# Kernel tuning notes

Hardware: AMD Instinct MI355X
Metric: run time of the kernel (lower is better)

## Reference

```python
import jax, jax.numpy as jnp
import numpy as np

N = 8192
NFEAT = 512
NHID = 256
NCLASS = 40
EDGE_P = 0.002  # ~16 avg degree


def setup_inputs() -> dict:
    key = jax.random.key(0)
    k1, k2, k3, k4 = jax.random.split(key, 4)
    x = jax.random.normal(k1, (N, NFEAT), dtype=jnp.float32)
    # unnormalized binary adjacency without self loops (module adds eye itself)
    adj = (jax.random.uniform(k2, (N, N)) < EDGE_P).astype(jnp.float32)
    # GCNConv weights: torch.rand(in, out) -> uniform[0,1)
    W1 = jax.random.uniform(k3, (NFEAT, NHID), dtype=jnp.float32)
    W2 = jax.random.uniform(k4, (NHID, NCLASS), dtype=jnp.float32)
    return {"x": x, "adj": adj, "W1": W1, "W2": W2}


def reference(x, adj, W1, W2):
    n = adj.shape[0]
    # add self loops: in_adj.to_dense() + eye
    A_hat = adj + jnp.eye(n, dtype=adj.dtype)
    # normalize_adj: D^{-1/2} A_hat D^{-1/2} (diag matmuls == row/col scaling)
    d = A_hat.sum(-1) ** -0.5  # [N]
    norm_adj = d[:, None] * A_hat * d[None, :]
    # conv1: relu(adj @ x @ W1); dropout is identity in eval mode
    h = jax.nn.relu((norm_adj @ x) @ W1)
    # conv2 reuses the same normalized adjacency (only one DGG layer by default)
    h2 = jax.nn.relu((norm_adj @ h) @ W2)
    return jax.nn.log_softmax(h2, axis=-1)
```

## Files before the change

### kernel.cpp

```cpp
#include <hip/hip_runtime.h>
#include <math.h>

#define NV 8192
#define CAP 64

typedef __attribute__((ext_vector_type(8))) short short8;
typedef __attribute__((ext_vector_type(4))) float f32x4;

static __device__ __forceinline__ unsigned short f2bf(float v) {
  unsigned int u = __float_as_uint(v);
  unsigned int r = (u + 0x7fffu + ((u >> 16) & 1u)) >> 16;
  return (unsigned short)r;
}
static __device__ __forceinline__ float bf2f(unsigned short h) {
  return __uint_as_float(((unsigned int)h) << 16);
}

__global__ __launch_bounds__(256) void mega_build_gemm1(
    const float* __restrict__ adj, const float* __restrict__ x,
    const float* __restrict__ W1, int* __restrict__ cols,
    int* __restrict__ rowcount, float* __restrict__ dinv,
    float* __restrict__ diagv, float* __restrict__ XW1) {
  __shared__ __align__(16) unsigned short sAh[128][40];
  __shared__ __align__(16) unsigned short sAl[128][40];
  __shared__ __align__(16) unsigned short sBh[64][40];
  __shared__ __align__(16) unsigned short sBl[64][40];
  __shared__ int cnt;
  __shared__ int diag_nz;
  __shared__ int wsum[4];

  int t = threadIdx.x;
  int lane = t & 63;

  if (blockIdx.x < 256) {
    const int K = 512;
    int b = blockIdx.x;
    int bn = (b & 3) * 64;
    int bm = (b >> 2) * 128;
    int w = t >> 6;
    int quad = lane >> 4, m16 = lane & 15;
    f32x4 acc[2][4] = {};
    for (int k0 = 0; k0 < K; k0 += 32) {
#pragma unroll
      for (int i = 0; i < 4; i++) {
        int id = t + i * 256;
        int row = id >> 3;
        int fq = id & 7;
        float4 v = *(const float4*)&x[(size_t)(bm + row) * K + k0 + fq * 4];
        ushort4 h, l;
        h.x = f2bf(v.x); l.x = f2bf(v.x - bf2f(h.x));
        h.y = f2bf(v.y); l.y = f2bf(v.y - bf2f(h.y));
        h.z = f2bf(v.z); l.z = f2bf(v.z - bf2f(h.z));
        h.w = f2bf(v.w); l.w = f2bf(v.w - bf2f(h.w));
        *(ushort4*)&sAh[row][fq * 4] = h;
        *(ushort4*)&sAl[row][fq * 4] = l;
      }
#pragma unroll
      for (int j = 0; j < 2; j++) {
        int id = t + j * 256;
        int k = id >> 4;
        int n4 = (id & 15) * 4;
        float4 v = *(const float4*)&W1[(size_t)(k0 + k) * 256 + bn + n4];
        float va[4] = {v.x, v.y, v.z, v.w};
#pragma unroll
        for (int c = 0; c < 4; c++) {
          unsigned short h = f2bf(va[c]);
          sBh[n4 + c][k] = h;
          sBl[n4 + c][k] = f2bf(va[c] - bf2f(h));
        }
      }
      __syncthreads();
      short8 ah[2], al[2], bh[4], bl[4];
#pragma unroll
      for (int i = 0; i < 2; i++) {
        ah[i] = *(const short8*)&sAh[w * 32 + i * 16 + m16][quad * 8];
        al[i] = *(const short8*)&sAl[w * 32 + i * 16 + m16][quad * 8];
      }
#pragma unroll
      for (int j = 0; j < 4; j++) {
        bh[j] = *(const short8*)&sBh[j * 16 + m16][quad * 8];
        bl[j] = *(const short8*)&sBl[j * 16 + m16][quad * 8];
      }
#pragma unroll
      for (int i = 0; i < 2; i++)
#pragma unroll
        for (int j = 0; j < 4; j++) {
          acc[i][j] = __builtin_amdgcn_mfma_f32_16x16x32_bf16(ah[i], bh[j], acc[i][j], 0, 0, 0);
          acc[i][j] = __builtin_amdgcn_mfma_f32_16x16x32_bf16(al[i], bh[j], acc[i][j], 0, 0, 0);
          acc[i][j] = __builtin_amdgcn_mfma_f32_16x16x32_bf16(ah[i], bl[j], acc[i][j], 0, 0, 0);
        }
      __syncthreads();
    }
#pragma unroll
    for (int i = 0; i < 2; i++)
#pragma unroll
      for (int j = 0; j < 4; j++)
#pragma unroll
        for (int r = 0; r < 4; r++)
          XW1[(size_t)(bm + w * 32 + i * 16 + quad * 4 + r) * 256 + bn + j * 16 + m16] =
              acc[i][j][r];
  } else {
    int row = blockIdx.x - 256;
    if (t == 0) { cnt = 0; diag_nz = 0; }
    __syncthreads();
    const float4* arow = (const float4*)(adj + (size_t)row * NV);
    float4 v0 = arow[t + 0 * 256];
    float4 v1 = arow[t + 1 * 256];
    float4 v2 = arow[t + 2 * 256];
    float4 v3 = arow[t + 3 * 256];
    float4 v4 = arow[t + 4 * 256];
    float4 v5 = arow[t + 5 * 256];
    float4 v6 = arow[t + 6 * 256];
    float4 v7 = arow[t + 7 * 256];
    int mycount = 0;
    float4 vv[8] = {v0, v1, v2, v3, v4, v5, v6, v7};
#pragma unroll
    for (int u = 0; u < 8; u++) {
      int i = t + u * 256;
      float va[4] = {vv[u].x, vv[u].y, vv[u].z, vv[u].w};
#pragma unroll
      for (int j = 0; j < 4; j++) {
        bool nz = (va[j] != 0.0f);
        mycount += nz ? 1 : 0;
        int c = i * 4 + j;
        bool isdiag = nz && (c == row);
        bool take = nz && !isdiag;
        if (isdiag) diag_nz = 1;
        unsigned long long m = __ballot(take);
        if (m != 0ull) {
          int tot = __popcll(m);
          int pre = __popcll(m & ((1ull << lane) - 1ull));
          int leader = __ffsll((unsigned long long)m) - 1;
          int base = 0;
          if (lane == leader) base = atomicAdd(&cnt, tot);
          base = __shfl(base, leader, 64);
          if (take) {
            int p = base + pre;
            if (p < CAP) cols[(size_t)row * CAP + p] = c;
          }
        }
      }
    }
    for (int off = 32; off > 0; off >>= 1) mycount += __shfl_xor(mycount, off, 64);
    if (lane == 0) wsum[t >> 6] = mycount;
    __syncthreads();
    if (t == 0) {
      int nnz = wsum[0] + wsum[1] + wsum[2] + wsum[3];
      float deg = (float)nnz + 1.0f;
      dinv[row] = 1.0f / sqrtf(deg);
      diagv[row] = diag_nz ? 2.0f : 1.0f;
      rowcount[row] = cnt > CAP ? CAP : cnt;
    }
  }
}

__global__ __launch_bounds__(256) void spmm_relu_k(
    const float* __restrict__ Z, const int* __restrict__ cols,
    const int* __restrict__ rowcount, const float* __restrict__ dinv,
    const float* __restrict__ diagv, float* __restrict__ H) {
  int lane = threadIdx.x & 63;
  int row = blockIdx.x * 4 + (threadIdx.x >> 6);
  const float4* Zr = (const float4*)Z;
  float di = dinv[row];
  float4 z = Zr[(size_t)row * 64 + lane];
  float dd = diagv[row] * di;
  float4 acc;
  acc.x = dd * z.x; acc.y = dd * z.y; acc.z = dd * z.z; acc.w = dd * z.w;
  int cnt = rowcount[row];
  const int* cr = cols + (size_t)row * CAP;
  int e = 0;
  for (; e + 8 <= cnt; e += 8) {
    int c0 = cr[e + 0], c1 = cr[e + 1], c2 = cr[e + 2], c3 = cr[e + 3];
    int c4 = cr[e + 4], c5 = cr[e + 5], c6 = cr[e + 6], c7 = cr[e + 7];
    float w0 = dinv[c0], w1 = dinv[c1], w2 = dinv[c2], w3 = dinv[c3];
    float w4 = dinv[c4], w5 = dinv[c5], w6 = dinv[c6], w7 = dinv[c7];
    float4 g0 = Zr[(size_t)c0 * 64 + lane];
    float4 g1 = Zr[(size_t)c1 * 64 + lane];
    float4 g2 = Zr[(size_t)c2 * 64 + lane];
    float4 g3 = Zr[(size_t)c3 * 64 + lane];
    float4 g4 = Zr[(size_t)c4 * 64 + lane];
    float4 g5 = Zr[(size_t)c5 * 64 + lane];
    float4 g6 = Zr[(size_t)c6 * 64 + lane];
    float4 g7 = Zr[(size_t)c7 * 64 + lane];
    acc.x += w0 * g0.x + w1 * g1.x + w2 * g2.x + w3 * g3.x;
    acc.y += w0 * g0.y + w1 * g1.y + w2 * g2.y + w3 * g3.y;
    acc.z += w0 * g0.z + w1 * g1.z + w2 * g2.z + w3 * g3.z;
    acc.w += w0 * g0.w + w1 * g1.w + w2 * g2.w + w3 * g3.w;
    acc.x += w4 * g4.x + w5 * g5.x + w6 * g6.x + w7 * g7.x;
    acc.y += w4 * g4.y + w5 * g5.y + w6 * g6.y + w7 * g7.y;
    acc.z += w4 * g4.z + w5 * g5.z + w6 * g6.z + w7 * g7.z;
    acc.w += w4 * g4.w + w5 * g5.w + w6 * g6.w + w7 * g7.w;
  }
  for (; e + 4 <= cnt; e += 4) {
    int c0 = cr[e + 0], c1 = cr[e + 1], c2 = cr[e + 2], c3 = cr[e + 3];
    float w0 = dinv[c0], w1 = dinv[c1], w2 = dinv[c2], w3 = dinv[c3];
    float4 g0 = Zr[(size_t)c0 * 64 + lane];
    float4 g1 = Zr[(size_t)c1 * 64 + lane];
    float4 g2 = Zr[(size_t)c2 * 64 + lane];
    float4 g3 = Zr[(size_t)c3 * 64 + lane];
    acc.x += w0 * g0.x + w1 * g1.x + w2 * g2.x + w3 * g3.x;
    acc.y += w0 * g0.y + w1 * g1.y + w2 * g2.y + w3 * g3.y;
    acc.z += w0 * g0.z + w1 * g1.z + w2 * g2.z + w3 * g3.z;
    acc.w += w0 * g0.w + w1 * g1.w + w2 * g2.w + w3 * g3.w;
  }
  for (; e < cnt; e++) {
    int c = cr[e];
    float w = dinv[c];
    float4 g = Zr[(size_t)c * 64 + lane];
    acc.x += w * g.x; acc.y += w * g.y; acc.z += w * g.z; acc.w += w * g.w;
  }
  float4 o;
  o.x = fmaxf(acc.x * di, 0.0f);
  o.y = fmaxf(acc.y * di, 0.0f);
  o.z = fmaxf(acc.z * di, 0.0f);
  o.w = fmaxf(acc.w * di, 0.0f);
  ((float4*)H)[(size_t)row * 64 + lane] = o;
}

__global__ __launch_bounds__(256) void gemm2_mfma(
    const float* __restrict__ H, const float* __restrict__ W2,
    float* __restrict__ HW2) {
  const int K = 256;
  __shared__ __align__(16) unsigned short sAh[32][40];
  __shared__ __align__(16) unsigned short sAl[32][40];
  __shared__ __align__(16) unsigned short sBh[64][40];
  __shared__ __align__(16) unsigned short sBl[64][40];
  int t = threadIdx.x;
  int bm = blockIdx.x * 32;
  int lane = t & 63, w = t >> 6;
  int quad = lane >> 4, m16 = lane & 15;
  int i = w & 1;
  int jj = (w >> 1) * 2;
  f32x4 acc[2] = {};
  for (int k0 = 0; k0 < K; k0 += 32) {
    {
      int row = t >> 3;
      int fq = t & 7;
      float4 v = *(const float4*)&H[(size_t)(bm + row) * K + k0 + fq * 4];
      ushort4 h, l;
      h.x = f2bf(v.x); l.x = f2bf(v.x - bf2f(h.x));
      h.y = f2bf(v.y); l.y = f2bf(v.y - bf2f(h.y));
      h.z = f2bf(v.z); l.z = f2bf(v.z - bf2f(h.z));
      h.w = f2bf(v.w); l.w = f2bf(v.w - bf2f(h.w));
      *(ushort4*)&sAh[row][fq * 4] = h;
      *(ushort4*)&sAl[row][fq * 4] = l;
    }
#pragma unroll
    for (int j = 0; j < 2; j++) {
      int id = t + j * 256;
      int k = id >> 4;
      int n4 = (id & 15) * 4;
#pragma unroll
      for (int c = 0; c < 4; c++) {
        float v = (n4 + c < 40) ? W2[(size_t)(k0 + k) * 40 + n4 + c] : 0.0f;
        unsigned short h = f2bf(v);
        sBh[n4 + c][k] = h;
        sBl[n4 + c][k] = f2bf(v - bf2f(h));
      }
    }
    __syncthreads();
    short8 ah = *(const short8*)&sAh[i * 16 + m16][quad * 8];
    short8 al = *(const short8*)&sAl[i * 16 + m16][quad * 8];
#pragma unroll
    for (int jx = 0; jx < 2; jx++) {
      short8 bh = *(const short8*)&sBh[(jj + jx) * 16 + m16][quad * 8];
      short8 bl = *(const short8*)&sBl[(jj + jx) * 16 + m16][quad * 8];
      acc[jx] = __builtin_amdgcn_mfma_f32_16x16x32_bf16(ah, bh, acc[jx], 0, 0, 0);
      acc[jx] = __builtin_amdgcn_mfma_f32_16x16x32_bf16(al, bh, acc[jx], 0, 0, 0);
      acc[jx] = __builtin_amdgcn_mfma_f32_16x16x32_bf16(ah, bl, acc[jx], 0, 0, 0);
    }
    __syncthreads();
  }
#pragma unroll
  for (int jx = 0; jx < 2; jx++)
#pragma unroll
    for (int r = 0; r < 4; r++)
      HW2[(size_t)(bm + i * 16 + quad * 4 + r) * 64 + (jj + jx) * 16 + m16] =
          acc[jx][r];
}

__global__ __launch_bounds__(256) void spmm2_lsm_k(
    const float* __restrict__ Z, const int* __restrict__ cols,
    const int* __restrict__ rowcount, const float* __restrict__ dinv,
    const float* __restrict__ diagv, float* __restrict__ out) {
  int lane = threadIdx.x & 63;
  int row = blockIdx.x * 4 + (threadIdx.x >> 6);
  float di = dinv[row];
  float acc = diagv[row] * di * Z[(size_t)row * 64 + lane];
  int cnt = rowcount[row];
  const int* cr = cols + (size_t)row * CAP;
  int e = 0;
  for (; e + 8 <= cnt; e += 8) {
    int c0 = cr[e + 0], c1 = cr[e + 1], c2 = cr[e + 2], c3 = cr[e + 3];
    int c4 = cr[e + 4], c5 = cr[e + 5], c6 = cr[e + 6], c7 = cr[e + 7];
    float w0 = dinv[c0], w1 = dinv[c1], w2 = dinv[c2], w3 = dinv[c3];
    float w4 = dinv[c4], w5 = dinv[c5], w6 = dinv[c6], w7 = dinv[c7];
    float g0 = Z[(size_t)c0 * 64 + lane];
    float g1 = Z[(size_t)c1 * 64 + lane];
    float g2 = Z[(size_t)c2 * 64 + lane];
    float g3 = Z[(size_t)c3 * 64 + lane];
    float g4 = Z[(size_t)c4 * 64 + lane];
    float g5 = Z[(size_t)c5 * 64 + lane];
    float g6 = Z[(size_t)c6 * 64 + lane];
    float g7 = Z[(size_t)c7 * 64 + lane];
    acc += w0 * g0 + w1 * g1 + w2 * g2 + w3 * g3;
    acc += w4 * g4 + w5 * g5 + w6 * g6 + w7 * g7;
  }
  for (; e + 4 <= cnt; e += 4) {
    int c0 = cr[e + 0], c1 = cr[e + 1], c2 = cr[e + 2], c3 = cr[e + 3];
    float w0 = dinv[c0], w1 = dinv[c1], w2 = dinv[c2], w3 = dinv[c3];
    acc += w0 * Z[(size_t)c0 * 64 + lane] + w1 * Z[(size_t)c1 * 64 + lane] +
           w2 * Z[(size_t)c2 * 64 + lane] + w3 * Z[(size_t)c3 * 64 + lane];
  }
  for (; e < cnt; e++) {
    int c = cr[e];
    acc += dinv[c] * Z[(size_t)c * 64 + lane];
  }
  float h2 = (lane < 40) ? fmaxf(acc * di, 0.0f) : -INFINITY;
  float m = h2;
  for (int off = 32; off > 0; off >>= 1) m = fmaxf(m, __shfl_xor(m, off, 64));
  float ex = (lane < 40) ? expf(h2 - m) : 0.0f;
  float s = ex;
  for (int off = 32; off > 0; off >>= 1) s += __shfl_xor(s, off, 64);
  float ls = logf(s);
  if (lane < 40) out[(size_t)row * 40 + lane] = h2 - m - ls;
}

extern "C" void kernel_launch(void* const* d_in, const int* in_sizes, int n_in,
                              void* d_out, int out_size, void* d_ws, size_t ws_size,
                              hipStream_t stream) {
  (void)in_sizes; (void)n_in; (void)out_size; (void)ws_size;
  const float* x   = (const float*)d_in[0];
  const float* adj = (const float*)d_in[1];
  const float* W1  = (const float*)d_in[2];
  const float* W2  = (const float*)d_in[3];
  float* out = (float*)d_out;
  char* ws = (char*)d_ws;

  int*   cols     = (int*)(ws);
  int*   rowcount = (int*)(ws + 2097152);
  float* dinv     = (float*)(ws + 2129920);
  float* diagv    = (float*)(ws + 2162688);
  float* XW1      = (float*)(ws + 2195456);
  float* H        = (float*)(ws + 10584064);
  float* HW2      = (float*)(ws + 18972672);

  hipLaunchKernelGGL(mega_build_gemm1, dim3(256 + NV), dim3(256), 0, stream,
                     adj, x, W1, cols, rowcount, dinv, diagv, XW1);
  hipLaunchKernelGGL(spmm_relu_k, dim3(NV / 4), dim3(256), 0, stream,
                     XW1, cols, rowcount, dinv, diagv, H);
  hipLaunchKernelGGL(gemm2_mfma, dim3(NV / 32), dim3(256), 0, stream,
                     H, W2, HW2);
  hipLaunchKernelGGL(spmm2_lsm_k, dim3(NV / 4), dim3(256), 0, stream,
                     HW2, cols, rowcount, dinv, diagv, out);
}
```

Measured before the change: 411.5 us.

## Halve GEMM1 tile height and replace per-element ballots with bitmask scan compaction

The XW1 GEMM now uses 64-row tiles instead of 128, doubling the GEMM block count to 512 and cutting LDS and register use per block. The adjacency row scan no longer does a ballot plus shuffle plus LDS atomic for each of the 32 elements per thread. Each thread instead builds a 32-bit mask of its nonzeros, a wave prefix scan gives its write offsets, and one atomic per wave reserves space. The degree is now taken from the compacted count plus the diagonal flag, and the order of column indices within a row changes.

```diff
diff --git a/kernel.cpp b/kernel.cpp
--- a/kernel.cpp
+++ b/kernel.cpp
@@ -21,28 +21,27 @@
     const float* __restrict__ W1, int* __restrict__ cols,
     int* __restrict__ rowcount, float* __restrict__ dinv,
     float* __restrict__ diagv, float* __restrict__ XW1) {
-  __shared__ __align__(16) unsigned short sAh[128][40];
-  __shared__ __align__(16) unsigned short sAl[128][40];
+  __shared__ __align__(16) unsigned short sAh[64][40];
+  __shared__ __align__(16) unsigned short sAl[64][40];
   __shared__ __align__(16) unsigned short sBh[64][40];
   __shared__ __align__(16) unsigned short sBl[64][40];
   __shared__ int cnt;
   __shared__ int diag_nz;
-  __shared__ int wsum[4];
 
   int t = threadIdx.x;
   int lane = t & 63;
 
-  if (blockIdx.x < 256) {
+  if (blockIdx.x < 512) {
     const int K = 512;
     int b = blockIdx.x;
     int bn = (b & 3) * 64;
-    int bm = (b >> 2) * 128;
+    int bm = (b >> 2) * 64;
     int w = t >> 6;
     int quad = lane >> 4, m16 = lane & 15;
-    f32x4 acc[2][4] = {};
+    f32x4 acc[4] = {};
     for (int k0 = 0; k0 < K; k0 += 32) {
 #pragma unroll
-      for (int i = 0; i < 4; i++) {
+      for (int i = 0; i < 2; i++) {
         int id = t + i * 256;
         int row = id >> 3;
         int fq = id & 7;
@@ -70,83 +69,74 @@
         }
       }
       __syncthreads();
-      short8 ah[2], al[2], bh[4], bl[4];
-#pragma unroll
-      for (int i = 0; i < 2; i++) {
-        ah[i] = *(const short8*)&sAh[w * 32 + i * 16 + m16][quad * 8];
-        al[i] = *(const short8*)&sAl[w * 32 + i * 16 + m16][quad * 8];
-      }
+      short8 ah = *(const short8*)&sAh[w * 16 + m16][quad * 8];
+      short8 al = *(const short8*)&sAl[w * 16 + m16][quad * 8];
 #pragma unroll
       for (int j = 0; j < 4; j++) {
-        bh[j] = *(const short8*)&sBh[j * 16 + m16][quad * 8];
-        bl[j] = *(const short8*)&sBl[j * 16 + m16][quad * 8];
-      }
-#pragma unroll
-      for (int i = 0; i < 2; i++)
-#pragma unroll
-        for (int j = 0; j < 4; j++) {
-          acc[i][j] = __builtin_amdgcn_mfma_f32_16x16x32_bf16(ah[i], bh[j], acc[i][j], 0, 0, 0);
-          acc[i][j] = __builtin_amdgcn_mfma_f32_16x16x32_bf16(al[i], bh[j], acc[i][j], 0, 0, 0);
-          acc[i][j] = __builtin_amdgcn_mfma_f32_16x16x32_bf16(ah[i], bl[j], acc[i][j], 0, 0, 0);
-        }
+        short8 bh = *(const short8*)&sBh[j * 16 + m16][quad * 8];
+        short8 bl = *(const short8*)&sBl[j * 16 + m16][quad * 8];
+        acc[j] = __builtin_amdgcn_mfma_f32_16x16x32_bf16(ah, bh, acc[j], 0, 0, 0);
+        acc[j] = __builtin_amdgcn_mfma_f32_16x16x32_bf16(al, bh, acc[j], 0, 0, 0);
+        acc[j] = __builtin_amdgcn_mfma_f32_16x16x32_bf16(ah, bl, acc[j], 0, 0, 0);
+      }
       __syncthreads();
     }
 #pragma unroll
-    for (int i = 0; i < 2; i++)
-#pragma unroll
-      for (int j = 0; j < 4; j++)
-#pragma unroll
-        for (int r = 0; r < 4; r++)
-          XW1[(size_t)(bm + w * 32 + i * 16 + quad * 4 + r) * 256 + bn + j * 16 + m16] =
-              acc[i][j][r];
+    for (int j = 0; j < 4; j++)
+#pragma unroll
+      for (int r = 0; r < 4; r++)
+        XW1[(size_t)(bm + w * 16 + quad * 4 + r) * 256 + bn + j * 16 + m16] =
+            acc[j][r];
   } else {
-    int row = blockIdx.x - 256;
+    int row = blockIdx.x - 512;
     if (t == 0) { cnt = 0; diag_nz = 0; }
     __syncthreads();
     const float4* arow = (const float4*)(adj + (size_t)row * NV);
-    float4 v0 = arow[t + 0 * 256];
-    float4 v1 = arow[t + 1 * 256];
-    float4 v2 = arow[t + 2 * 256];
-    float4 v3 = arow[t + 3 * 256];
-    float4 v4 = arow[t + 4 * 256];
-    float4 v5 = arow[t + 5 * 256];
-    float4 v6 = arow[t + 6 * 256];
-    float4 v7 = arow[t + 7 * 256];
-    int mycount = 0;
-    float4 vv[8] = {v0, v1, v2, v3, v4, v5, v6, v7};
+    float4 vv[8];
+    vv[0] = arow[t + 0 * 256];
+    vv[1] = arow[t + 1 * 256];
+    vv[2] = arow[t + 2 * 256];
+    vv[3] = arow[t + 3 * 256];
+    vv[4] = arow[t + 4 * 256];
+    vv[5] = arow[t + 5 * 256];
+    vv[6] = arow[t + 6 * 256];
+    vv[7] = arow[t + 7 * 256];
+    unsigned int wm = 0;
 #pragma unroll
     for (int u = 0; u < 8; u++) {
-      int i = t + u * 256;
       float va[4] = {vv[u].x, vv[u].y, vv[u].z, vv[u].w};
 #pragma unroll
       for (int j = 0; j < 4; j++) {
         bool nz = (va[j] != 0.0f);
-        mycount += nz ? 1 : 0;
-        int c = i * 4 + j;
-        bool isdiag = nz && (c == row);
-        bool take = nz && !isdiag;
-        if (isdiag) diag_nz = 1;
-        unsigned long long m = __ballot(take);
-        if (m != 0ull) {
-          int tot = __popcll(m);
-          int pre = __popcll(m & ((1ull << lane) - 1ull));
-          int leader = __ffsll((unsigned long long)m) - 1;
-          int base = 0;
-          if (lane == leader) base = atomicAdd(&cnt, tot);
-          base = __shfl(base, leader, 64);
-          if (take) {
-            int p = base + pre;
-            if (p < CAP) cols[(size_t)row * CAP + p] = c;
-          }
+        int c = 4 * t + (u << 10) + j;
+        if (nz) {
+          if (c == row) diag_nz = 1;
+          else wm |= 1u << (u * 4 + j);
         }
       }
     }
-    for (int off = 32; off > 0; off >>= 1) mycount += __shfl_xor(mycount, off, 64);
-    if (lane == 0) wsum[t >> 6] = mycount;
+    int myc = __popc(wm);
+    int pre = myc;
+#pragma unroll
+    for (int off = 1; off < 64; off <<= 1) {
+      int nb = __shfl_up(pre, off, 64);
+      if (lane >= off) pre += nb;
+    }
+    int wtot = __shfl(pre, 63, 64);
+    int base = 0;
+    if (lane == 63) base = atomicAdd(&cnt, wtot);
+    base = __shfl(base, 63, 64);
+    int p0 = base + (pre - myc);
+    while (wm) {
+      int p = __ffs(wm) - 1;
+      wm &= wm - 1;
+      int c = 4 * t + ((p >> 2) << 10) + (p & 3);
+      if (p0 < CAP) cols[(size_t)row * CAP + p0] = c;
+      p0++;
+    }
     __syncthreads();
     if (t == 0) {
-      int nnz = wsum[0] + wsum[1] + wsum[2] + wsum[3];
-      float deg = (float)nnz + 1.0f;
+      float deg = (float)(cnt + diag_nz) + 1.0f;
       dinv[row] = 1.0f / sqrtf(deg);
       diagv[row] = diag_nz ? 2.0f : 1.0f;
       rowcount[row] = cnt > CAP ? CAP : cnt;
@@ -345,7 +335,7 @@
   float* H        = (float*)(ws + 10584064);
   float* HW2      = (float*)(ws + 18972672);
 
-  hipLaunchKernelGGL(mega_build_gemm1, dim3(256 + NV), dim3(256), 0, stream,
+  hipLaunchKernelGGL(mega_build_gemm1, dim3(512 + NV), dim3(256), 0, stream,
                      adj, x, W1, cols, rowcount, dinv, diagv, XW1);
   hipLaunchKernelGGL(spmm_relu_k, dim3(NV / 4), dim3(256), 0, stream,
                      XW1, cols, rowcount, dinv, diagv, H);
```

After: 407.5 us. About the same (-1.0%).
